# Optimization experiments

Hardware: AMD Instinct MI355X
Metric: run time of the kernel (lower is better)

The kernel has to match this reference:

```python
import jax, jax.numpy as jnp
import numpy as np

S = 8          # num_slots
DSLOT = 128    # slot_dim
D_IN = 768     # input feature dim
ITERS = 3      # slot_att_iter
RES = 21       # 336 // 16
NGRID = RES * RES   # 441 grid positions
NTOK = 441          # tokens kept per frame (no drop here)
NFRAME = 2
F_ = 2 * NFRAME + 1  # 5 frames per clip
CLIPS = 8
B = CLIPS * F_       # 40
SIGMA = 5.0
SCALE = DSLOT ** -0.5
EPS = 1e-8


def layernorm(x, g, b):
    m = x.mean(-1, keepdims=True)
    v = ((x - m) ** 2).mean(-1, keepdims=True)
    return (x - m) * jax.lax.rsqrt(v + 1e-5) * g + b


def setup_inputs() -> dict:
    key = jax.random.key(0)
    ks = iter(jax.random.split(key, 64))
    def nrm(shape, s=0.02):
        return jax.random.normal(next(ks), shape, jnp.float32) * s
    xs = jnp.linspace(-1.0, 1.0, RES)
    ys = jnp.linspace(-1.0, 1.0, RES)
    gx, gy = jnp.meshgrid(xs, ys)  # indexing='xy' as in torch
    abs_grid = jnp.stack([gx.ravel(), gy.ravel()], axis=-1)  # [NGRID, 2]
    return {
        "inputs": jax.random.normal(next(ks), (B, NTOK, D_IN), jnp.float32),
        "token_indices": jnp.sort(jax.random.randint(next(ks), (B, NTOK), 0, NGRID), axis=-1),
        "abs_grid": abs_grid,
        "slots_init": nrm((1, S, DSLOT), 0.1),
        "S_p_init": nrm((1, S, 1, 2), 0.02),
        "S_s_init": jax.random.uniform(next(ks), (1, S, 1, 2), jnp.float32, 0.3, 0.7),
        "WQ": nrm((DSLOT, DSLOT)), "ln_g": jnp.ones((DSLOT,)), "ln_b": jnp.zeros((DSLOT,)),
        "gru_w_ih": nrm((DSLOT, 3 * DSLOT)), "gru_w_hh": nrm((DSLOT, 3 * DSLOT)),
        "gru_b_ih": jnp.zeros((3 * DSLOT,)), "gru_b_hh": jnp.zeros((3 * DSLOT,)),
        "mlp_ln_g": jnp.ones((DSLOT,)), "mlp_ln_b": jnp.zeros((DSLOT,)),
        "mlp_w1": nrm((DSLOT, 4 * DSLOT)), "mlp_b1": jnp.zeros((4 * DSLOT,)),
        "mlp_w2": nrm((4 * DSLOT, DSLOT)), "mlp_b2": jnp.zeros((DSLOT,)),
        "WK": nrm((DSLOT, DSLOT)), "WV": nrm((DSLOT, DSLOT)),
        "Wg": nrm((2, DSLOT)), "bg": jnp.zeros((DSLOT,)),
        "Wf1": nrm((DSLOT, DSLOT)), "bf1": jnp.zeros((DSLOT,)),
        "Wf2": nrm((DSLOT, DSLOT)), "bf2": jnp.zeros((DSLOT,)),
        "im_ln1_g": jnp.ones((D_IN,)), "im_ln1_b": jnp.zeros((D_IN,)),
        "im_w1": nrm((D_IN, D_IN)), "im_b1": jnp.zeros((D_IN,)),
        "im_w2": nrm((D_IN, DSLOT)), "im_b2": jnp.zeros((DSLOT,)),
        "im_ln2_g": jnp.ones((DSLOT,)), "im_ln2_b": jnp.zeros((DSLOT,)),
        "fin_w": nrm((DSLOT, DSLOT)), "fin_b": jnp.zeros((DSLOT,)),
    }


def _forward(inputs, token_indices, abs_grid, slots_init, S_p_init, S_s_init,
             WQ, ln_g, ln_b, gru_w_ih, gru_w_hh, gru_b_ih, gru_b_hh,
             mlp_ln_g, mlp_ln_b, mlp_w1, mlp_b1, mlp_w2, mlp_b2,
             WK, WV, Wg, bg, Wf1, bf1, Wf2, bf2,
             im_ln1_g, im_ln1_b, im_w1, im_b1, im_w2, im_b2, im_ln2_g, im_ln2_b,
             fin_w, fin_b):
    Bb = inputs.shape[0]
    # initial_mlp: LN -> Linear -> ReLU -> Linear -> LN
    x = layernorm(inputs, im_ln1_g, im_ln1_b)
    x = jax.nn.relu(x @ im_w1 + im_b1)
    x = x @ im_w2 + im_b2
    x = layernorm(x, im_ln2_g, im_ln2_b)          # [B, N, Dslot]
    # K/V projections of inputs are slot-independent; compute once.
    Kx = x @ WK                                    # [B, N, Dslot]
    Vx = x @ WV
    ag = abs_grid[token_indices]                   # [B, N, 2] per-batch gather
    slots = jnp.broadcast_to(slots_init, (Bb, S, DSLOT))
    S_p = jnp.broadcast_to(S_p_init, (Bb, S, 1, 2))
    S_s = jnp.broadcast_to(S_s_init, (Bb, S, 1, 2))

    def f_net(z):  # f = Linear -> ReLU -> Linear
        return jax.nn.relu(z @ Wf1 + bf1) @ Wf2 + bf2

    attn = None
    for t in range(ITERS + 1):
        slots_prev = slots
        sn = layernorm(slots, ln_g, ln_b)
        rel = (ag[:, None] - S_p) / (S_s * SIGMA)  # [B, S, N, 2]
        gr = rel @ Wg + bg                          # [B, S, N, Dslot]
        k = f_net(Kx[:, None] + gr)
        v = f_net(Vx[:, None] + gr)
        q = sn @ WQ                                 # [B, S, Dslot]
        dots = jnp.einsum('bsd,bsjd->bsj', q, k) * SCALE
        attn = jax.nn.softmax(dots, axis=1) + EPS   # softmax over slots
        attn = attn / attn.sum(-1, keepdims=True)   # renormalize over tokens
        updates = jnp.einsum('bsjd,bsj->bsd', v, attn)
        S_p = jnp.einsum('bjd,bsj->bsd', ag, attn)[:, :, None, :]
        S_s = jnp.sqrt(jnp.einsum('bsjd,bsj->bsd', (ag[:, None] - S_p) ** 2, attn))[:, :, None, :]
        if t != ITERS:
            # torch GRUCell
            xg = updates.reshape(-1, DSLOT)
            hg = slots_prev.reshape(-1, DSLOT)
            gi = xg @ gru_w_ih + gru_b_ih
            gh = hg @ gru_w_hh + gru_b_hh
            i_r, i_z, i_n = jnp.split(gi, 3, axis=-1)
            h_r, h_z, h_n = jnp.split(gh, 3, axis=-1)
            r = jax.nn.sigmoid(i_r + h_r)
            z = jax.nn.sigmoid(i_z + h_z)
            n = jnp.tanh(i_n + r * h_n)
            slots = ((1.0 - z) * n + z * hg).reshape(Bb, S, DSLOT)
            # residual pre-LN MLP (dropout is identity in eval)
            y = layernorm(slots, mlp_ln_g, mlp_ln_b)
            y = jax.nn.relu(y @ mlp_w1 + mlp_b1) @ mlp_w2 + mlp_b2
            slots = slots + y
    slots = slots @ fin_w + fin_b
    attn_out = attn.reshape(-1, F_, S, NTOK)[:, NFRAME]  # center frame
    return slots, attn_out


def reference(inputs, token_indices, abs_grid, slots_init, S_p_init, S_s_init,
              WQ, ln_g, ln_b, gru_w_ih, gru_w_hh, gru_b_ih, gru_b_hh,
              mlp_ln_g, mlp_ln_b, mlp_w1, mlp_b1, mlp_w2, mlp_b2,
              WK, WV, Wg, bg, Wf1, bf1, Wf2, bf2,
              im_ln1_g, im_ln1_b, im_w1, im_b1, im_w2, im_b2, im_ln2_g, im_ln2_b,
              fin_w, fin_b):
    return _forward(inputs, token_indices, abs_grid, slots_init, S_p_init, S_s_init,
                    WQ, ln_g, ln_b, gru_w_ih, gru_w_hh, gru_b_ih, gru_b_hh,
                    mlp_ln_g, mlp_ln_b, mlp_w1, mlp_b1, mlp_w2, mlp_b2,
                    WK, WV, Wg, bg, Wf1, bf1, Wf2, bf2,
                    im_ln1_g, im_ln1_b, im_w1, im_b1, im_w2, im_b2, im_ln2_g, im_ln2_b,
                    fin_w, fin_b)
```

## Files before the change

### kernel.cpp

```cpp
#include <hip/hip_runtime.h>
#include <cstdio>

#define NB 40
#define NS 8
#define NT 441
#define DIN 768
#define DD 128
#define NTOT (NB*NT)
#define FSCALE 0.08838834764831843f

typedef short s8v __attribute__((ext_vector_type(8)));
typedef float f4v __attribute__((ext_vector_type(4)));

__device__ inline ushort f2bf(float f){
  unsigned u = __float_as_uint(f);
  unsigned r = (u + 0x7fffu + ((u >> 16) & 1u)) >> 16;
  return (ushort)r;
}
__device__ inline float bf2f(ushort h){ return __uint_as_float(((unsigned)h) << 16); }

struct PP {
  const float *inputs; const int *tok_idx; const float *abs_grid;
  const float *slots_init, *Sp_init, *Ss_init;
  const float *WQ, *ln_g, *ln_b;
  const float *gru_w_ih, *gru_w_hh, *gru_b_ih, *gru_b_hh;
  const float *mlp_ln_g, *mlp_ln_b, *mlp_w1, *mlp_b1, *mlp_w2, *mlp_b2;
  const float *WK, *WV, *Wg, *bg, *Wf1, *bf1, *Wf2, *bf2;
  const float *im_ln1_g, *im_ln1_b, *im_w1, *im_b1, *im_w2, *im_b2, *im_ln2_g, *im_ln2_b;
  const float *fin_w, *fin_b;
  float *x, *A_K, *A_V, *WKf, *WVf, *Wg1, *c1, *Wf2T;
  float *slots_g, *qw_g, *qb_g, *spss_g, *hpart_g, *a_g;
  ushort *xnh, *xnl, *hh, *hl, *W1Th, *W1Tl, *W2Th, *W2Tl;
  float *out;
};

__global__ __launch_bounds__(128) void prep_weights(PP p){
  int r = blockIdx.x, d = threadIdx.x;
  float accK = 0.f, accV = 0.f;
  for (int kk = 0; kk < DD; kk++){
    float w = p.Wf1[kk*DD + d];
    accK = fmaf(p.WK[r*DD+kk], w, accK);
    accV = fmaf(p.WV[r*DD+kk], w, accV);
  }
  p.WKf[r*DD+d] = accK; p.WVf[r*DD+d] = accV;
  if (r < 2){
    float a = 0.f;
    for (int kk = 0; kk < DD; kk++) a = fmaf(p.Wg[r*DD+kk], p.Wf1[kk*DD+d], a);
    p.Wg1[r*DD+d] = a;
  }
  if (r == 2){
    float a = 0.f;
    for (int kk = 0; kk < DD; kk++) a = fmaf(p.bg[kk], p.Wf1[kk*DD+d], a);
    p.c1[d] = a + p.bf1[d];
  }
  p.Wf2T[d*DD + r] = p.Wf2[r*DD + d];
}

__global__ __launch_bounds__(256) void transpose_split(const float* __restrict__ W,
                                                       ushort* __restrict__ WTh,
                                                       ushort* __restrict__ WTl,
                                                       int K, int N){
  __shared__ float tile[64][65];
  int tid = threadIdx.x;
  int k0 = blockIdx.x * 64, n0 = blockIdx.y * 64;
  #pragma unroll
  for (int i = 0; i < 4; i++){
    int k = i*16 + (tid >> 4);
    int n4 = (tid & 15) * 4;
    float4 v = *(const float4*)(W + (long)(k0+k)*N + n0 + n4);
    tile[k][n4+0] = v.x; tile[k][n4+1] = v.y; tile[k][n4+2] = v.z; tile[k][n4+3] = v.w;
  }
  __syncthreads();
  #pragma unroll
  for (int i = 0; i < 4; i++){
    int n = i*16 + (tid >> 4);
    int k4 = (tid & 15) * 4;
    ushort4 h4, l4;
    float v0 = tile[k4+0][n], v1 = tile[k4+1][n], v2 = tile[k4+2][n], v3 = tile[k4+3][n];
    h4.x = f2bf(v0); l4.x = f2bf(v0 - bf2f(h4.x));
    h4.y = f2bf(v1); l4.y = f2bf(v1 - bf2f(h4.y));
    h4.z = f2bf(v2); l4.z = f2bf(v2 - bf2f(h4.z));
    h4.w = f2bf(v3); l4.w = f2bf(v3 - bf2f(h4.w));
    *(ushort4*)(WTh + (long)(n0+n)*K + k0 + k4) = h4;
    *(ushort4*)(WTl + (long)(n0+n)*K + k0 + k4) = l4;
  }
}

__global__ __launch_bounds__(256) void ln1_split(PP p){
  int tok = blockIdx.x*4 + (threadIdx.x >> 6);
  int l = threadIdx.x & 63;
  const float* src = p.inputs + (long)tok*DIN;
  float4 v[3];
  float s = 0.f, s2 = 0.f;
  #pragma unroll
  for (int pp = 0; pp < 3; pp++){
    v[pp] = *(const float4*)(src + pp*256 + l*4);
    s  += v[pp].x + v[pp].y + v[pp].z + v[pp].w;
    s2 += v[pp].x*v[pp].x + v[pp].y*v[pp].y + v[pp].z*v[pp].z + v[pp].w*v[pp].w;
  }
  #pragma unroll
  for (int m = 1; m < 64; m <<= 1){ s += __shfl_xor(s, m); s2 += __shfl_xor(s2, m); }
  float mean = s*(1.f/DIN), var = s2*(1.f/DIN) - mean*mean;
  float rstd = rsqrtf(var + 1e-5f);
  #pragma unroll
  for (int pp = 0; pp < 3; pp++){
    int idx = pp*256 + l*4;
    float4 g = *(const float4*)(p.im_ln1_g + idx);
    float4 b = *(const float4*)(p.im_ln1_b + idx);
    float y0 = (v[pp].x-mean)*rstd*g.x + b.x;
    float y1 = (v[pp].y-mean)*rstd*g.y + b.y;
    float y2 = (v[pp].z-mean)*rstd*g.z + b.z;
    float y3 = (v[pp].w-mean)*rstd*g.w + b.w;
    ushort4 h4, l4;
    h4.x = f2bf(y0); l4.x = f2bf(y0 - bf2f(h4.x));
    h4.y = f2bf(y1); l4.y = f2bf(y1 - bf2f(h4.y));
    h4.z = f2bf(y2); l4.z = f2bf(y2 - bf2f(h4.z));
    h4.w = f2bf(y3); l4.w = f2bf(y3 - bf2f(h4.w));
    *(ushort4*)(p.xnh + (long)tok*DIN + idx) = h4;
    *(ushort4*)(p.xnl + (long)tok*DIN + idx) = l4;
  }
}

__global__ __launch_bounds__(256) void gemm1_128(PP p){
  __shared__ __align__(16) ushort As[2][128][40];
  __shared__ __align__(16) ushort Bs[2][128][40];
  int id = blockIdx.x;
  int xcd = id & 7, idx = id >> 3;
  int m_t = xcd + 8*(idx/6), n_t = idx % 6;
  if (m_t >= 138) return;
  int m0 = m_t*128, n0 = n_t*128;
  int tid = threadIdx.x;
  int w = tid >> 6, lane = tid & 63;
  int wm = w >> 1, wn = w & 1;
  f4v acc[4][4];
  #pragma unroll
  for (int mf = 0; mf < 4; mf++)
    #pragma unroll
    for (int nf = 0; nf < 4; nf++) acc[mf][nf] = (f4v)(0.f);

  for (int kb = 0; kb < DIN; kb += 32){
    __syncthreads();
    #pragma unroll
    for (int i = 0; i < 4; i++){
      int c = tid + i*256;
      int s = c >> 9, rem = c & 511;
      int r = rem >> 2, kg = rem & 3;
      int gr = min(m0 + r, NTOT-1);
      const float4 va = *(const float4*)((s ? p.xnl : p.xnh) + (long)gr*DIN + kb + kg*8);
      *(float4*)(&As[s][r][kg*8]) = va;
      const float4 vb = *(const float4*)((s ? p.W1Tl : p.W1Th) + (long)(n0 + r)*DIN + kb + kg*8);
      *(float4*)(&Bs[s][r][kg*8]) = vb;
    }
    __syncthreads();
    int kg = lane >> 4, rA = lane & 15;
    s8v a0[4], a1[4], b0[4], b1[4];
    #pragma unroll
    for (int mf = 0; mf < 4; mf++){
      a0[mf] = *(const s8v*)(&As[0][wm*64 + mf*16 + rA][kg*8]);
      a1[mf] = *(const s8v*)(&As[1][wm*64 + mf*16 + rA][kg*8]);
    }
    #pragma unroll
    for (int nf = 0; nf < 4; nf++){
      b0[nf] = *(const s8v*)(&Bs[0][wn*64 + nf*16 + rA][kg*8]);
      b1[nf] = *(const s8v*)(&Bs[1][wn*64 + nf*16 + rA][kg*8]);
    }
    #pragma unroll
    for (int mf = 0; mf < 4; mf++)
      #pragma unroll
      for (int nf = 0; nf < 4; nf++){
        acc[mf][nf] = __builtin_amdgcn_mfma_f32_16x16x32_bf16(a0[mf], b0[nf], acc[mf][nf], 0, 0, 0);
        acc[mf][nf] = __builtin_amdgcn_mfma_f32_16x16x32_bf16(a0[mf], b1[nf], acc[mf][nf], 0, 0, 0);
        acc[mf][nf] = __builtin_amdgcn_mfma_f32_16x16x32_bf16(a1[mf], b0[nf], acc[mf][nf], 0, 0, 0);
      }
  }

  int rbase = (lane >> 4) * 4, cn = lane & 15;
  #pragma unroll
  for (int mf = 0; mf < 4; mf++)
    #pragma unroll
    for (int nf = 0; nf < 4; nf++){
      int n = n0 + wn*64 + nf*16 + cn;
      float bs = p.im_b1[n];
      #pragma unroll
      for (int r = 0; r < 4; r++){
        int m = m0 + wm*64 + mf*16 + rbase + r;
        if (m < NTOT){
          float v = fmaxf(acc[mf][nf][r] + bs, 0.f);
          ushort h = f2bf(v);
          p.hh[(long)m*DIN + n] = h;
          p.hl[(long)m*DIN + n] = f2bf(v - bf2f(h));
        }
      }
    }
}

__global__ __launch_bounds__(256) void gemm_split2(
    const ushort* __restrict__ Ah, const ushort* __restrict__ Al,
    const ushort* __restrict__ Bh, const ushort* __restrict__ Bl,
    const float* __restrict__ bias,
    float* __restrict__ Xout, const float* __restrict__ g2, const float* __restrict__ b2,
    int M)
{
  __shared__ __align__(16) char smemc[64*132*4];
  ushort* As = (ushort*)smemc;
  ushort* Bs = (ushort*)(smemc + 10240);
  int tid = threadIdx.x;
  int n0 = blockIdx.x * 128, m0 = blockIdx.y * 64;
  int w = tid >> 6, lane = tid & 63;
  f4v acc[4][2];
  #pragma unroll
  for (int mf = 0; mf < 4; mf++)
    #pragma unroll
    for (int nf = 0; nf < 2; nf++) acc[mf][nf] = (f4v)(0.f);

  for (int kb = 0; kb < DIN; kb += 32){
    __syncthreads();
    #pragma unroll
    for (int i = 0; i < 2; i++){
      int c = tid + i*256;
      int s = c >> 8, r = (c >> 2) & 63, kg = c & 3;
      int gr = min(m0 + r, M-1);
      const float4 va = *(const float4*)((s ? Al : Ah) + (long)gr*DIN + kb + kg*8);
      *(float4*)(As + s*2560 + r*40 + kg*8) = va;
    }
    #pragma unroll
    for (int i = 0; i < 4; i++){
      int c = tid + i*256;
      int s = c >> 9, r = (c >> 2) & 127, kg = c & 3;
      const float4 vb = *(const float4*)((s ? Bl : Bh) + (long)(n0 + r)*DIN + kb + kg*8);
      *(float4*)(Bs + s*5120 + r*40 + kg*8) = vb;
    }
    __syncthreads();
    int kg = lane >> 4, rA = lane & 15;
    s8v a0[4], a1[4], b0[2], b1[2];
    #pragma unroll
    for (int mf = 0; mf < 4; mf++){
      a0[mf] = *(const s8v*)(As +        (mf*16 + rA)*40 + kg*8);
      a1[mf] = *(const s8v*)(As + 2560 + (mf*16 + rA)*40 + kg*8);
    }
    #pragma unroll
    for (int nf = 0; nf < 2; nf++){
      int rb = w*32 + nf*16 + rA;
      b0[nf] = *(const s8v*)(Bs +        rb*40 + kg*8);
      b1[nf] = *(const s8v*)(Bs + 5120 + rb*40 + kg*8);
    }
    #pragma unroll
    for (int mf = 0; mf < 4; mf++)
      #pragma unroll
      for (int nf = 0; nf < 2; nf++){
        acc[mf][nf] = __builtin_amdgcn_mfma_f32_16x16x32_bf16(a0[mf], b0[nf], acc[mf][nf], 0, 0, 0);
        acc[mf][nf] = __builtin_amdgcn_mfma_f32_16x16x32_bf16(a0[mf], b1[nf], acc[mf][nf], 0, 0, 0);
        acc[mf][nf] = __builtin_amdgcn_mfma_f32_16x16x32_bf16(a1[mf], b0[nf], acc[mf][nf], 0, 0, 0);
      }
  }

  int rbase = (lane >> 4) * 4, cn = lane & 15;
  __syncthreads();
  float* Dl = (float*)smemc;
  #pragma unroll
  for (int mf = 0; mf < 4; mf++)
    #pragma unroll
    for (int nf = 0; nf < 2; nf++){
      int n = w*32 + nf*16 + cn;
      float bs = bias[n];
      #pragma unroll
      for (int r = 0; r < 4; r++)
        Dl[(mf*16 + rbase + r)*132 + n] = acc[mf][nf][r] + bs;
    }
  __syncthreads();
  for (int rr = 0; rr < 16; rr++){
    int row = w*16 + rr;
    float e0 = Dl[row*132 + lane], e1 = Dl[row*132 + 64 + lane];
    float s = e0 + e1, s2 = e0*e0 + e1*e1;
    #pragma unroll
    for (int m2 = 1; m2 < 64; m2 <<= 1){ s += __shfl_xor(s, m2); s2 += __shfl_xor(s2, m2); }
    float mean = s*(1.f/DD), var = s2*(1.f/DD) - mean*mean;
    float rstd = rsqrtf(var + 1e-5f);
    int m = m0 + row;
    if (m < M){
      Xout[(long)m*DD + lane]      = (e0-mean)*rstd*g2[lane]      + b2[lane];
      Xout[(long)m*DD + 64 + lane] = (e1-mean)*rstd*g2[64 + lane] + b2[64 + lane];
    }
  }
}

__global__ __launch_bounds__(256) void k2_proj(PP p){
  __shared__ float xt[32][132];
  int tid = threadIdx.x; int g0 = blockIdx.x * 32;
  for (int f = tid; f < 32*32; f += 256){
    int tok = f >> 5, pos = (f & 31) * 4;
    int gt = g0 + tok;
    float4 v = (gt < NTOT) ? *(const float4*)(p.x + (long)gt*DD + pos)
                           : make_float4(0.f,0.f,0.f,0.f);
    *(float4*)&xt[tok][pos] = v;
  }
  __syncthreads();
  int d = tid & 127, grp = tid >> 7;
  float aK[16], aV[16];
  float c1v = p.c1[d];
  #pragma unroll
  for (int t = 0; t < 16; t++){ aK[t] = c1v; aV[t] = c1v; }
  for (int kk = 0; kk < DD; kk += 4){
    float k0 = p.WKf[(kk+0)*DD+d], k1 = p.WKf[(kk+1)*DD+d], k2 = p.WKf[(kk+2)*DD+d], k3 = p.WKf[(kk+3)*DD+d];
    float v0 = p.WVf[(kk+0)*DD+d], v1 = p.WVf[(kk+1)*DD+d], v2 = p.WVf[(kk+2)*DD+d], v3 = p.WVf[(kk+3)*DD+d];
    #pragma unroll
    for (int t = 0; t < 16; t++){
      float4 xv = *(const float4*)&xt[grp*16+t][kk];
      aK[t] = fmaf(xv.x,k0, fmaf(xv.y,k1, fmaf(xv.z,k2, fmaf(xv.w,k3, aK[t]))));
      aV[t] = fmaf(xv.x,v0, fmaf(xv.y,v1, fmaf(xv.z,v2, fmaf(xv.w,v3, aV[t]))));
    }
  }
  #pragma unroll
  for (int t = 0; t < 16; t++){
    int gt = g0 + grp*16 + t;
    if (gt < NTOT){ p.A_K[(long)gt*DD+d] = aK[t]; p.A_V[(long)gt*DD+d] = aV[t]; }
  }
}

__device__ void phase0g(const PP& p, int bs, int tid, float* scr, const float* sl,
                        float Sp0, float Sp1, float Ss0, float Ss1){
  float* sn   = scr;
  float* qv   = scr + 128;
  float* part = scr + 256;
  float* red  = scr + 512;
  int o = tid & 127, h = tid >> 7;
  float v = (tid < 128) ? sl[tid] : 0.f;
  float s1 = v, s2 = v*v;
  #pragma unroll
  for (int m = 1; m < 64; m <<= 1){ s1 += __shfl_xor(s1,m); s2 += __shfl_xor(s2,m); }
  if (tid < 128 && (tid & 63) == 0){ red[(tid>>6)*2] = s1; red[(tid>>6)*2+1] = s2; }
  __syncthreads();
  float mean = (red[0]+red[2])*(1.f/128.f);
  float var  = (red[1]+red[3])*(1.f/128.f) - mean*mean;
  float rstd = rsqrtf(var + 1e-5f);
  if (tid < 128) sn[tid] = (v-mean)*rstd*p.ln_g[tid] + p.ln_b[tid];
  __syncthreads();
  float acc = 0.f;
  for (int k = 0; k < 64; k++) acc = fmaf(sn[h*64+k], p.WQ[(h*64+k)*128+o], acc);
  part[h*128+o] = acc;
  __syncthreads();
  if (tid < 128) qv[tid] = part[tid] + part[128+tid];
  __syncthreads();
  float acc2 = 0.f;
  for (int k = 0; k < 64; k++) acc2 = fmaf(qv[h*64+k], p.Wf2T[(h*64+k)*128+o], acc2);
  part[h*128+o] = acc2;
  __syncthreads();
  if (tid < 128) p.qw_g[(long)bs*128+tid] = part[tid] + part[128+tid];
  float pb = (tid < 128) ? qv[tid]*p.bf2[tid] : 0.f;
  #pragma unroll
  for (int m = 1; m < 64; m <<= 1) pb += __shfl_xor(pb,m);
  if ((tid & 63) == 0) red[4 + (tid>>6)] = pb;
  __syncthreads();
  if (tid == 0){
    p.qb_g[bs] = FSCALE*(red[4]+red[5]+red[6]+red[7]);
    p.spss_g[bs*4+0] = Sp0; p.spss_g[bs*4+1] = Sp1;
    p.spss_g[bs*4+2] = 1.f/(Ss0*5.0f); p.spss_g[bs*4+3] = 1.f/(Ss1*5.0f);
  }
}

__global__ __launch_bounds__(256) void k_init(PP p){
  __shared__ float sl[128];
  __shared__ float scr[520];
  int bs = blockIdx.x, ss = bs & 7, tid = threadIdx.x;
  if (tid < 128){
    float v = p.slots_init[ss*128+tid];
    sl[tid] = v;
    p.slots_g[(long)bs*128+tid] = v;
  }
  __syncthreads();
  phase0g(p, bs, tid, scr, sl,
          p.Sp_init[ss*2], p.Sp_init[ss*2+1], p.Ss_init[ss*2], p.Ss_init[ss*2+1]);
}

template<int LAST>
__global__ __launch_bounds__(256) void kA(PP p){
  int b = blockIdx.x / 7, tile = blockIdx.x % 7;
  int tid = threadIdx.x, wid = tid >> 6, lane = tid & 63;
  __shared__ float qws[8][132];
  __shared__ float qbs[8];
  __shared__ float spssL[32];
  __shared__ float agt[64][2];
  __shared__ float a_tile[8][64];
  __shared__ float hpartL[4][8][128];
  for (int f = tid; f < 8*128; f += 256){
    int s = f >> 7, d = f & 127;
    qws[s][(d&31)*4 + (d>>5)] = p.qw_g[((long)b*8+s)*128 + d];
  }
  if (tid < 8)  qbs[tid] = p.qb_g[b*8+tid];
  if (tid < 32) spssL[tid] = p.spss_g[b*32+tid];
  if (tid < 64){
    int j = tile*64 + tid;
    float g0 = 0.f, g1 = 0.f;
    if (j < NT){ int idx = p.tok_idx[b*NT+j]; g0 = p.abs_grid[idx*2]; g1 = p.abs_grid[idx*2+1]; }
    agt[tid][0] = g0; agt[tid][1] = g1;
  }
  __syncthreads();

  {
    int tl = lane >> 2, dg = lane & 3;
    int jtok = wid*16 + tl, j = tile*64 + jtok;
    bool valid = j < NT;
    int jc = valid ? j : 0;
    float aa[32], w0[32], w1[32];
    const float* src = p.A_K + ((long)(b*NT+jc))*DD + dg*32;
    #pragma unroll
    for (int i4 = 0; i4 < 8; i4++){
      float4 t = *(const float4*)(src + i4*4);
      aa[i4*4+0]=t.x; aa[i4*4+1]=t.y; aa[i4*4+2]=t.z; aa[i4*4+3]=t.w;
    }
    #pragma unroll
    for (int i4 = 0; i4 < 8; i4++){
      float4 t0 = *(const float4*)(p.Wg1 + dg*32 + i4*4);
      float4 t1 = *(const float4*)(p.Wg1 + DD + dg*32 + i4*4);
      w0[i4*4+0]=t0.x; w0[i4*4+1]=t0.y; w0[i4*4+2]=t0.z; w0[i4*4+3]=t0.w;
      w1[i4*4+0]=t1.x; w1[i4*4+1]=t1.y; w1[i4*4+2]=t1.z; w1[i4*4+3]=t1.w;
    }
    float ag0 = agt[jtok][0], ag1 = agt[jtok][1];
    float dv[8];
    #pragma unroll
    for (int s = 0; s < 8; s++){
      float rel0 = (ag0 - spssL[s*4+0])*spssL[s*4+2];
      float rel1 = (ag1 - spssL[s*4+1])*spssL[s*4+3];
      float acc = 0.f;
      #pragma unroll
      for (int i = 0; i < 32; i++){
        float hk = fmaxf(fmaf(rel0, w0[i], fmaf(rel1, w1[i], aa[i])), 0.f);
        acc = fmaf(hk, qws[s][i*4+dg], acc);
      }
      acc += __shfl_xor(acc, 1); acc += __shfl_xor(acc, 2);
      dv[s] = acc*FSCALE + qbs[s];
    }
    if (dg == 0){
      float m = -1e30f;
      #pragma unroll
      for (int s = 0; s < 8; s++) m = fmaxf(m, dv[s]);
      float tot = 0.f;
      #pragma unroll
      for (int s = 0; s < 8; s++){ dv[s] = expf(dv[s]-m); tot += dv[s]; }
      float inv = 1.f/tot;
      #pragma unroll
      for (int s = 0; s < 8; s++)
        a_tile[s][jtok] = valid ? (dv[s]*inv + 1e-8f) : 0.f;
    }
  }
  __syncthreads();

  #pragma unroll
  for (int si = 0; si < 2; si++){
    int s = wid*2 + si;
    float a = a_tile[s][lane];
    float g0 = agt[lane][0], g1 = agt[lane][1];
    float v0 = a, v1 = a*g0, v2 = a*g1, v3 = a*g0*g0, v4 = a*g1*g1;
    #pragma unroll
    for (int m = 1; m < 64; m <<= 1){
      v0 += __shfl_xor(v0,m); v1 += __shfl_xor(v1,m); v2 += __shfl_xor(v2,m);
      v3 += __shfl_xor(v3,m); v4 += __shfl_xor(v4,m);
    }
    if (lane == 0){
      float* st = p.hpart_g + ((long)(b*7+tile)*8 + s)*136 + 128;
      st[0]=v0; st[1]=v1; st[2]=v2; st[3]=v3; st[4]=v4;
    }
  }

  if (LAST){
    if ((b % 5) == 2){
      int clip = b/5;
      for (int f = tid; f < 8*64; f += 256){
        int s = f >> 6, jt = f & 63;
        int j = tile*64 + jt;
        if (j < NT) p.a_g[((long)clip*8 + s)*NT + j] = a_tile[s][jt];
      }
    }
    return;
  }

  {
    float sp0[8], sp1[8], si0[8], si1[8];
    #pragma unroll
    for (int s = 0; s < 8; s++){
      sp0[s]=spssL[s*4+0]; sp1[s]=spssL[s*4+1]; si0[s]=spssL[s*4+2]; si1[s]=spssL[s*4+3];
    }
    int d0 = lane, d1 = lane + 64;
    float wg0a = p.Wg1[d0], wg1a = p.Wg1[DD+d0];
    float wg0b = p.Wg1[d1], wg1b = p.Wg1[DD+d1];
    float acc0[8], acc1[8];
    #pragma unroll
    for (int s = 0; s < 8; s++){ acc0[s]=0.f; acc1[s]=0.f; }
    for (int jj = wid; jj < 64; jj += 4){
      int j = tile*64 + jj;
      if (j >= NT) continue;
      float av0 = p.A_V[((long)(b*NT+j))*DD + d0];
      float av1 = p.A_V[((long)(b*NT+j))*DD + d1];
      float g0 = agt[jj][0], g1 = agt[jj][1];
      #pragma unroll
      for (int s = 0; s < 8; s++){
        float rel0 = (g0 - sp0[s])*si0[s];
        float rel1 = (g1 - sp1[s])*si1[s];
        float a = a_tile[s][jj];
        float hv0 = fmaxf(fmaf(rel0, wg0a, fmaf(rel1, wg1a, av0)), 0.f);
        float hv1 = fmaxf(fmaf(rel0, wg0b, fmaf(rel1, wg1b, av1)), 0.f);
        acc0[s] = fmaf(a, hv0, acc0[s]);
        acc1[s] = fmaf(a, hv1, acc1[s]);
      }
    }
    #pragma unroll
    for (int s = 0; s < 8; s++){ hpartL[wid][s][d0] = acc0[s]; hpartL[wid][s][d1] = acc1[s]; }
    __syncthreads();
    for (int f = tid; f < 1024; f += 256){
      int s = f >> 7, d = f & 127;
      p.hpart_g[((long)(b*7+tile)*8 + s)*136 + d] =
        hpartL[0][s][d] + hpartL[1][s][d] + hpartL[2][s][d] + hpartL[3][s][d];
    }
  }
}

template<int LAST>
__global__ __launch_bounds__(256) void kB(PP p){
  __shared__ float red[8];
  __shared__ float sl[128];
  __shared__ float hb[128];
  __shared__ float scr[2304];
  int bs = blockIdx.x, b = bs >> 3, ss = bs & 7, tid = threadIdx.x;
  if (tid < 5){
    float v = 0.f;
    #pragma unroll
    for (int t7 = 0; t7 < 7; t7++) v += p.hpart_g[((long)(b*7+t7)*8 + ss)*136 + 128 + tid];
    red[tid] = v;
  }
  __syncthreads();
  float SA = red[0], inv = 1.f/SA;
  float Sp0 = red[1]*inv, Sp1 = red[2]*inv;
  float Ss0 = sqrtf(fmaxf(red[3]*inv - Sp0*Sp0, 0.f));
  float Ss1 = sqrtf(fmaxf(red[4]*inv - Sp1*Sp1, 0.f));

  if (LAST){
    if ((b % 5) == 2){
      int clip = b/5;
      long base = (long)NB*NS*DD + ((long)clip*8 + ss)*NT;
      const float* arow = p.a_g + ((long)clip*8 + ss)*NT;
      for (int j = tid; j < NT; j += 256) p.out[base+j] = arow[j]*inv;
    }
    if (tid < 128) sl[tid] = p.slots_g[(long)bs*128+tid];
    __syncthreads();
    int o = tid & 127, h = tid >> 7;
    float acc = 0.f;
    for (int k = 0; k < 64; k++) acc = fmaf(sl[h*64+k], p.fin_w[(h*64+k)*128+o], acc);
    scr[h*128+o] = acc;
    __syncthreads();
    if (tid < 128) p.out[(long)bs*128+tid] = p.fin_b[tid] + scr[tid] + scr[128+tid];
    return;
  }

  if (tid < 128){
    float v = 0.f;
    #pragma unroll
    for (int t7 = 0; t7 < 7; t7++) v += p.hpart_g[((long)(b*7+t7)*8 + ss)*136 + tid];
    hb[tid] = v * inv;
    sl[tid] = p.slots_g[(long)bs*128+tid];
  }
  __syncthreads();
  float* part = scr;
  float* upd  = scr + 256;
  float* gil  = scr + 384;
  float* ghl  = scr + 768;
  float* hnl  = scr + 1152;
  float* yv   = scr + 1280;
  float* h1   = scr + 1408;
  int o = tid & 127, h = tid >> 7;
  float acc2 = 0.f;
  for (int k = 0; k < 64; k++) acc2 = fmaf(hb[h*64+k], p.Wf2[(h*64+k)*128+o], acc2);
  part[h*128+o] = acc2;
  __syncthreads();
  if (tid < 128) upd[tid] = part[tid] + part[128+tid] + p.bf2[tid];
  __syncthreads();
  int oA = tid, oB = tid + 256;
  float giA = p.gru_b_ih[oA], ghA = p.gru_b_hh[oA];
  float giB = 0.f, ghB = 0.f;
  if (tid < 128){ giB = p.gru_b_ih[oB]; ghB = p.gru_b_hh[oB]; }
  for (int k = 0; k < 128; k++){
    float uk = upd[k], sk = sl[k];
    giA = fmaf(uk, p.gru_w_ih[k*384+oA], giA);
    ghA = fmaf(sk, p.gru_w_hh[k*384+oA], ghA);
    if (tid < 128){
      giB = fmaf(uk, p.gru_w_ih[k*384+oB], giB);
      ghB = fmaf(sk, p.gru_w_hh[k*384+oB], ghB);
    }
  }
  gil[oA] = giA; ghl[oA] = ghA;
  if (tid < 128){ gil[oB] = giB; ghl[oB] = ghB; }
  __syncthreads();
  float hnv = 0.f;
  if (tid < 128){
    float r = 1.f/(1.f+expf(-(gil[tid]+ghl[tid])));
    float z = 1.f/(1.f+expf(-(gil[128+tid]+ghl[128+tid])));
    float n = tanhf(gil[256+tid] + r*ghl[256+tid]);
    hnv = (1.f-z)*n + z*sl[tid];
  }
  float t1 = hnv, t2 = hnv*hnv;
  #pragma unroll
  for (int m = 1; m < 64; m <<= 1){ t1 += __shfl_xor(t1,m); t2 += __shfl_xor(t2,m); }
  if (tid < 128 && (tid & 63) == 0){ red[(tid>>6)*2] = t1; red[(tid>>6)*2+1] = t2; }
  __syncthreads();
  float mean = (red[0]+red[2])*(1.f/128.f);
  float var  = (red[1]+red[3])*(1.f/128.f) - mean*mean;
  float rstd = rsqrtf(var + 1e-5f);
  if (tid < 128){
    hnl[tid] = hnv;
    yv[tid] = (hnv-mean)*rstd*p.mlp_ln_g[tid] + p.mlp_ln_b[tid];
  }
  __syncthreads();
  float m1A = p.mlp_b1[tid], m1B = p.mlp_b1[tid+256];
  for (int k = 0; k < 128; k++){
    float y = yv[k];
    m1A = fmaf(y, p.mlp_w1[k*512+tid], m1A);
    m1B = fmaf(y, p.mlp_w1[k*512+tid+256], m1B);
  }
  h1[tid] = fmaxf(m1A, 0.f); h1[tid+256] = fmaxf(m1B, 0.f);
  __syncthreads();
  float a2 = 0.f;
  for (int kk = 0; kk < 256; kk++) a2 = fmaf(h1[h*256+kk], p.mlp_w2[(h*256+kk)*128+o], a2);
  part[h*128+o] = a2;
  __syncthreads();
  if (tid < 128){
    float sln = hnl[tid] + p.mlp_b2[tid] + part[tid] + part[128+tid];
    sl[tid] = sln;
    p.slots_g[(long)bs*128+tid] = sln;
  }
  __syncthreads();
  phase0g(p, bs, tid, scr, sl, Sp0, Sp1, Ss0, Ss1);
}

extern "C" void kernel_launch(void* const* d_in, const int* in_sizes, int n_in,
                              void* d_out, int out_size, void* d_ws, size_t ws_size,
                              hipStream_t stream){
  PP p;
  p.inputs=(const float*)d_in[0]; p.tok_idx=(const int*)d_in[1]; p.abs_grid=(const float*)d_in[2];
  p.slots_init=(const float*)d_in[3]; p.Sp_init=(const float*)d_in[4]; p.Ss_init=(const float*)d_in[5];
  p.WQ=(const float*)d_in[6]; p.ln_g=(const float*)d_in[7]; p.ln_b=(const float*)d_in[8];
  p.gru_w_ih=(const float*)d_in[9]; p.gru_w_hh=(const float*)d_in[10];
  p.gru_b_ih=(const float*)d_in[11]; p.gru_b_hh=(const float*)d_in[12];
  p.mlp_ln_g=(const float*)d_in[13]; p.mlp_ln_b=(const float*)d_in[14];
  p.mlp_w1=(const float*)d_in[15]; p.mlp_b1=(const float*)d_in[16];
  p.mlp_w2=(const float*)d_in[17]; p.mlp_b2=(const float*)d_in[18];
  p.WK=(const float*)d_in[19]; p.WV=(const float*)d_in[20]; p.Wg=(const float*)d_in[21]; p.bg=(const float*)d_in[22];
  p.Wf1=(const float*)d_in[23]; p.bf1=(const float*)d_in[24]; p.Wf2=(const float*)d_in[25]; p.bf2=(const float*)d_in[26];
  p.im_ln1_g=(const float*)d_in[27]; p.im_ln1_b=(const float*)d_in[28];
  p.im_w1=(const float*)d_in[29]; p.im_b1=(const float*)d_in[30];
  p.im_w2=(const float*)d_in[31]; p.im_b2=(const float*)d_in[32];
  p.im_ln2_g=(const float*)d_in[33]; p.im_ln2_b=(const float*)d_in[34];
  p.fin_w=(const float*)d_in[35]; p.fin_b=(const float*)d_in[36];

  float* w = (float*)d_ws;
  size_t need = 0;
  auto alloc = [&](size_t nfl){ nfl = (nfl + 3) & ~(size_t)3; float* r = w + need; need += nfl; return r; };
  p.x    = alloc((size_t)NTOT*DD);
  p.A_K  = alloc((size_t)NTOT*DD);
  p.A_V  = alloc((size_t)NTOT*DD);
  p.WKf  = alloc(DD*DD);
  p.WVf  = alloc(DD*DD);
  p.Wg1  = alloc(2*DD);
  p.c1   = alloc(DD);
  p.Wf2T = alloc(DD*DD);
  p.slots_g = alloc(320*128);
  p.qw_g    = alloc(320*128);
  p.qb_g    = alloc(320);
  p.spss_g  = alloc(320*4);
  p.hpart_g = alloc((size_t)280*8*136);
  p.a_g     = alloc((size_t)8*8*NT);
  p.xnh  = (ushort*)alloc((size_t)NTOT*DIN/2);
  p.xnl  = (ushort*)alloc((size_t)NTOT*DIN/2);
  p.hh   = (ushort*)alloc((size_t)NTOT*DIN/2);
  p.hl   = (ushort*)alloc((size_t)NTOT*DIN/2);
  p.W1Th = (ushort*)alloc((size_t)DIN*DIN/2);
  p.W1Tl = (ushort*)alloc((size_t)DIN*DIN/2);
  p.W2Th = (ushort*)alloc((size_t)DD*DIN/2);
  p.W2Tl = (ushort*)alloc((size_t)DD*DIN/2);
  p.out = (float*)d_out;
  if (ws_size < need*sizeof(float)){
    fprintf(stderr, "kernel_launch: ws too small (%zu < %zu)\n", ws_size, need*sizeof(float));
    return;
  }

  prep_weights<<<dim3(DD), dim3(128), 0, stream>>>(p);
  transpose_split<<<dim3(DIN/64, DIN/64), dim3(256), 0, stream>>>(p.im_w1, p.W1Th, p.W1Tl, DIN, DIN);
  transpose_split<<<dim3(DIN/64, DD/64), dim3(256), 0, stream>>>(p.im_w2, p.W2Th, p.W2Tl, DIN, DD);
  ln1_split<<<dim3(NTOT/4), dim3(256), 0, stream>>>(p);
  gemm1_128<<<dim3(832), dim3(256), 0, stream>>>(p);
  gemm_split2<<<dim3(1, (NTOT+63)/64), dim3(256), 0, stream>>>(
      p.hh, p.hl, p.W2Th, p.W2Tl, p.im_b2,
      p.x, p.im_ln2_g, p.im_ln2_b, NTOT);
  k2_proj<<<dim3((NTOT+31)/32), dim3(256), 0, stream>>>(p);
  k_init<<<dim3(320), dim3(256), 0, stream>>>(p);

  for (int t = 0; t < 3; t++){
    kA<0><<<dim3(NB*7), dim3(256), 0, stream>>>(p);
    kB<0><<<dim3(320), dim3(256), 0, stream>>>(p);
  }
  kA<1><<<dim3(NB*7), dim3(256), 0, stream>>>(p);
  kB<1><<<dim3(320), dim3(256), 0, stream>>>(p);
}
```

Before: 461.6 us.

## Fuse LN2 and K/V projection into GEMM2 epilogue using split-bf16 MFMA

The second input-MLP GEMM now applies LayerNorm in its epilogue and immediately projects the normalized rows through the fused K/V weights with split-bf16 MFMA. This removes the fp32 x round trip and the separate scalar k2_proj kernel. Weight prep now writes transposed hi/lo bf16 copies of the fused K/V weights. The two transposes are merged into one launch, and slot init is folded into the LN1 kernel as extra blocks, cutting launch count. The cost is 68KB of dynamic shared memory per GEMM2 block, which limits occupancy, plus the K/V weights being read straight from global memory.

```diff
diff --git a/kernel.cpp b/kernel.cpp
--- a/kernel.cpp
+++ b/kernel.cpp
@@ -28,9 +28,10 @@
   const float *WK, *WV, *Wg, *bg, *Wf1, *bf1, *Wf2, *bf2;
   const float *im_ln1_g, *im_ln1_b, *im_w1, *im_b1, *im_w2, *im_b2, *im_ln2_g, *im_ln2_b;
   const float *fin_w, *fin_b;
-  float *x, *A_K, *A_V, *WKf, *WVf, *Wg1, *c1, *Wf2T;
+  float *A_K, *A_V, *Wg1, *c1, *Wf2T;
   float *slots_g, *qw_g, *qb_g, *spss_g, *hpart_g, *a_g;
   ushort *xnh, *xnl, *hh, *hl, *W1Th, *W1Tl, *W2Th, *W2Tl;
+  ushort *WKfTh, *WKfTl, *WVfTh, *WVfTl;
   float *out;
 };
 
@@ -42,7 +43,9 @@
     accK = fmaf(p.WK[r*DD+kk], w, accK);
     accV = fmaf(p.WV[r*DD+kk], w, accV);
   }
-  p.WKf[r*DD+d] = accK; p.WVf[r*DD+d] = accV;
+  ushort hk = f2bf(accK), hv = f2bf(accV);
+  p.WKfTh[d*DD + r] = hk; p.WKfTl[d*DD + r] = f2bf(accK - bf2f(hk));
+  p.WVfTh[d*DD + r] = hv; p.WVfTl[d*DD + r] = f2bf(accV - bf2f(hv));
   if (r < 2){
     float a = 0.f;
     for (int kk = 0; kk < DD; kk++) a = fmaf(p.Wg[r*DD+kk], p.Wf1[kk*DD+d], a);
@@ -56,13 +59,13 @@
   p.Wf2T[d*DD + r] = p.Wf2[r*DD + d];
 }
 
-__global__ __launch_bounds__(256) void transpose_split(const float* __restrict__ W,
-                                                       ushort* __restrict__ WTh,
-                                                       ushort* __restrict__ WTl,
-                                                       int K, int N){
+__global__ __launch_bounds__(256) void transpose_both(PP p){
   __shared__ float tile[64][65];
+  int t = blockIdx.x;
+  const float* W; ushort *WTh, *WTl; int N, k0, n0;
+  if (t < 144){ W = p.im_w1; WTh = p.W1Th; WTl = p.W1Tl; N = 768; k0 = (t/12)*64; n0 = (t%12)*64; }
+  else { t -= 144; W = p.im_w2; WTh = p.W2Th; WTl = p.W2Tl; N = 128; k0 = (t/2)*64; n0 = (t&1)*64; }
   int tid = threadIdx.x;
-  int k0 = blockIdx.x * 64, n0 = blockIdx.y * 64;
   #pragma unroll
   for (int i = 0; i < 4; i++){
     int k = i*16 + (tid >> 4);
@@ -81,43 +84,98 @@
     h4.y = f2bf(v1); l4.y = f2bf(v1 - bf2f(h4.y));
     h4.z = f2bf(v2); l4.z = f2bf(v2 - bf2f(h4.z));
     h4.w = f2bf(v3); l4.w = f2bf(v3 - bf2f(h4.w));
-    *(ushort4*)(WTh + (long)(n0+n)*K + k0 + k4) = h4;
-    *(ushort4*)(WTl + (long)(n0+n)*K + k0 + k4) = l4;
-  }
-}
-
-__global__ __launch_bounds__(256) void ln1_split(PP p){
-  int tok = blockIdx.x*4 + (threadIdx.x >> 6);
-  int l = threadIdx.x & 63;
-  const float* src = p.inputs + (long)tok*DIN;
-  float4 v[3];
-  float s = 0.f, s2 = 0.f;
-  #pragma unroll
-  for (int pp = 0; pp < 3; pp++){
-    v[pp] = *(const float4*)(src + pp*256 + l*4);
-    s  += v[pp].x + v[pp].y + v[pp].z + v[pp].w;
-    s2 += v[pp].x*v[pp].x + v[pp].y*v[pp].y + v[pp].z*v[pp].z + v[pp].w*v[pp].w;
-  }
-  #pragma unroll
-  for (int m = 1; m < 64; m <<= 1){ s += __shfl_xor(s, m); s2 += __shfl_xor(s2, m); }
-  float mean = s*(1.f/DIN), var = s2*(1.f/DIN) - mean*mean;
+    *(ushort4*)(WTh + (long)(n0+n)*DIN + k0 + k4) = h4;
+    *(ushort4*)(WTl + (long)(n0+n)*DIN + k0 + k4) = l4;
+  }
+}
+
+__device__ void phase0g(const PP& p, int bs, int tid, float* scr, const float* sl,
+                        float Sp0, float Sp1, float Ss0, float Ss1){
+  float* sn   = scr;
+  float* qv   = scr + 128;
+  float* part = scr + 256;
+  float* red  = scr + 512;
+  int o = tid & 127, h = tid >> 7;
+  float v = (tid < 128) ? sl[tid] : 0.f;
+  float s1 = v, s2 = v*v;
+  #pragma unroll
+  for (int m = 1; m < 64; m <<= 1){ s1 += __shfl_xor(s1,m); s2 += __shfl_xor(s2,m); }
+  if (tid < 128 && (tid & 63) == 0){ red[(tid>>6)*2] = s1; red[(tid>>6)*2+1] = s2; }
+  __syncthreads();
+  float mean = (red[0]+red[2])*(1.f/128.f);
+  float var  = (red[1]+red[3])*(1.f/128.f) - mean*mean;
   float rstd = rsqrtf(var + 1e-5f);
-  #pragma unroll
-  for (int pp = 0; pp < 3; pp++){
-    int idx = pp*256 + l*4;
-    float4 g = *(const float4*)(p.im_ln1_g + idx);
-    float4 b = *(const float4*)(p.im_ln1_b + idx);
-    float y0 = (v[pp].x-mean)*rstd*g.x + b.x;
-    float y1 = (v[pp].y-mean)*rstd*g.y + b.y;
-    float y2 = (v[pp].z-mean)*rstd*g.z + b.z;
-    float y3 = (v[pp].w-mean)*rstd*g.w + b.w;
-    ushort4 h4, l4;
-    h4.x = f2bf(y0); l4.x = f2bf(y0 - bf2f(h4.x));
-    h4.y = f2bf(y1); l4.y = f2bf(y1 - bf2f(h4.y));
-    h4.z = f2bf(y2); l4.z = f2bf(y2 - bf2f(h4.z));
-    h4.w = f2bf(y3); l4.w = f2bf(y3 - bf2f(h4.w));
-    *(ushort4*)(p.xnh + (long)tok*DIN + idx) = h4;
-    *(ushort4*)(p.xnl + (long)tok*DIN + idx) = l4;
+  if (tid < 128) sn[tid] = (v-mean)*rstd*p.ln_g[tid] + p.ln_b[tid];
+  __syncthreads();
+  float acc = 0.f;
+  for (int k = 0; k < 64; k++) acc = fmaf(sn[h*64+k], p.WQ[(h*64+k)*128+o], acc);
+  part[h*128+o] = acc;
+  __syncthreads();
+  if (tid < 128) qv[tid] = part[tid] + part[128+tid];
+  __syncthreads();
+  float acc2 = 0.f;
+  for (int k = 0; k < 64; k++) acc2 = fmaf(qv[h*64+k], p.Wf2T[(h*64+k)*128+o], acc2);
+  part[h*128+o] = acc2;
+  __syncthreads();
+  if (tid < 128) p.qw_g[(long)bs*128+tid] = part[tid] + part[128+tid];
+  float pb = (tid < 128) ? qv[tid]*p.bf2[tid] : 0.f;
+  #pragma unroll
+  for (int m = 1; m < 64; m <<= 1) pb += __shfl_xor(pb,m);
+  if ((tid & 63) == 0) red[4 + (tid>>6)] = pb;
+  __syncthreads();
+  if (tid == 0){
+    p.qb_g[bs] = FSCALE*(red[4]+red[5]+red[6]+red[7]);
+    p.spss_g[bs*4+0] = Sp0; p.spss_g[bs*4+1] = Sp1;
+    p.spss_g[bs*4+2] = 1.f/(Ss0*5.0f); p.spss_g[bs*4+3] = 1.f/(Ss1*5.0f);
+  }
+}
+
+__global__ __launch_bounds__(256) void ln1_init(PP p){
+  __shared__ float sl[128];
+  __shared__ float scr[520];
+  if (blockIdx.x < 4410){
+    int tok = blockIdx.x*4 + (threadIdx.x >> 6);
+    int l = threadIdx.x & 63;
+    const float* src = p.inputs + (long)tok*DIN;
+    float4 v[3];
+    float s = 0.f, s2 = 0.f;
+    #pragma unroll
+    for (int pp = 0; pp < 3; pp++){
+      v[pp] = *(const float4*)(src + pp*256 + l*4);
+      s  += v[pp].x + v[pp].y + v[pp].z + v[pp].w;
+      s2 += v[pp].x*v[pp].x + v[pp].y*v[pp].y + v[pp].z*v[pp].z + v[pp].w*v[pp].w;
+    }
+    #pragma unroll
+    for (int m = 1; m < 64; m <<= 1){ s += __shfl_xor(s, m); s2 += __shfl_xor(s2, m); }
+    float mean = s*(1.f/DIN), var = s2*(1.f/DIN) - mean*mean;
+    float rstd = rsqrtf(var + 1e-5f);
+    #pragma unroll
+    for (int pp = 0; pp < 3; pp++){
+      int idx = pp*256 + l*4;
+      float4 g = *(const float4*)(p.im_ln1_g + idx);
+      float4 b = *(const float4*)(p.im_ln1_b + idx);
+      float y0 = (v[pp].x-mean)*rstd*g.x + b.x;
+      float y1 = (v[pp].y-mean)*rstd*g.y + b.y;
+      float y2 = (v[pp].z-mean)*rstd*g.z + b.z;
+      float y3 = (v[pp].w-mean)*rstd*g.w + b.w;
+      ushort4 h4, l4;
+      h4.x = f2bf(y0); l4.x = f2bf(y0 - bf2f(h4.x));
+      h4.y = f2bf(y1); l4.y = f2bf(y1 - bf2f(h4.y));
+      h4.z = f2bf(y2); l4.z = f2bf(y2 - bf2f(h4.z));
+      h4.w = f2bf(y3); l4.w = f2bf(y3 - bf2f(h4.w));
+      *(ushort4*)(p.xnh + (long)tok*DIN + idx) = h4;
+      *(ushort4*)(p.xnl + (long)tok*DIN + idx) = l4;
+    }
+  } else {
+    int bs = blockIdx.x - 4410, ss = bs & 7, tid = threadIdx.x;
+    if (tid < 128){
+      float v = p.slots_init[ss*128+tid];
+      sl[tid] = v;
+      p.slots_g[(long)bs*128+tid] = v;
+    }
+    __syncthreads();
+    phase0g(p, bs, tid, scr, sl,
+            p.Sp_init[ss*2], p.Sp_init[ss*2+1], p.Ss_init[ss*2], p.Ss_init[ss*2+1]);
   }
 }
 
@@ -194,19 +252,15 @@
     }
 }
 
-__global__ __launch_bounds__(256) void gemm_split2(
-    const ushort* __restrict__ Ah, const ushort* __restrict__ Al,
-    const ushort* __restrict__ Bh, const ushort* __restrict__ Bl,
-    const float* __restrict__ bias,
-    float* __restrict__ Xout, const float* __restrict__ g2, const float* __restrict__ b2,
-    int M)
-{
-  __shared__ __align__(16) char smemc[64*132*4];
-  ushort* As = (ushort*)smemc;
-  ushort* Bs = (ushort*)(smemc + 10240);
-  int tid = threadIdx.x;
-  int n0 = blockIdx.x * 128, m0 = blockIdx.y * 64;
-  int w = tid >> 6, lane = tid & 63;
+__global__ __launch_bounds__(256) void gemm2_fused(PP p){
+  extern __shared__ __align__(16) char smem[];
+  ushort* As = (ushort*)smem;
+  ushort* Bs = (ushort*)(smem + 10240);
+  float*  Dl = (float*)smem;
+  ushort* xsh = (ushort*)(smem + 33792);
+  ushort* xsl = (ushort*)(smem + 33792 + 17408);
+  int m0 = blockIdx.x * 64;
+  int tid = threadIdx.x, w = tid >> 6, lane = tid & 63;
   f4v acc[4][2];
   #pragma unroll
   for (int mf = 0; mf < 4; mf++)
@@ -219,15 +273,15 @@
     for (int i = 0; i < 2; i++){
       int c = tid + i*256;
       int s = c >> 8, r = (c >> 2) & 63, kg = c & 3;
-      int gr = min(m0 + r, M-1);
-      const float4 va = *(const float4*)((s ? Al : Ah) + (long)gr*DIN + kb + kg*8);
+      int gr = min(m0 + r, NTOT-1);
+      const float4 va = *(const float4*)((s ? p.hl : p.hh) + (long)gr*DIN + kb + kg*8);
       *(float4*)(As + s*2560 + r*40 + kg*8) = va;
     }
     #pragma unroll
     for (int i = 0; i < 4; i++){
       int c = tid + i*256;
       int s = c >> 9, r = (c >> 2) & 127, kg = c & 3;
-      const float4 vb = *(const float4*)((s ? Bl : Bh) + (long)(n0 + r)*DIN + kb + kg*8);
+      const float4 vb = *(const float4*)((s ? p.W2Tl : p.W2Th) + (long)r*DIN + kb + kg*8);
       *(float4*)(Bs + s*5120 + r*40 + kg*8) = vb;
     }
     __syncthreads();
@@ -256,13 +310,12 @@
 
   int rbase = (lane >> 4) * 4, cn = lane & 15;
   __syncthreads();
-  float* Dl = (float*)smemc;
   #pragma unroll
   for (int mf = 0; mf < 4; mf++)
     #pragma unroll
     for (int nf = 0; nf < 2; nf++){
       int n = w*32 + nf*16 + cn;
-      float bs = bias[n];
+      float bs = p.im_b2[n];
       #pragma unroll
       for (int r = 0; r < 4; r++)
         Dl[(mf*16 + rbase + r)*132 + n] = acc[mf][nf][r] + bs;
@@ -276,100 +329,49 @@
     for (int m2 = 1; m2 < 64; m2 <<= 1){ s += __shfl_xor(s, m2); s2 += __shfl_xor(s2, m2); }
     float mean = s*(1.f/DD), var = s2*(1.f/DD) - mean*mean;
     float rstd = rsqrtf(var + 1e-5f);
-    int m = m0 + row;
-    if (m < M){
-      Xout[(long)m*DD + lane]      = (e0-mean)*rstd*g2[lane]      + b2[lane];
-      Xout[(long)m*DD + 64 + lane] = (e1-mean)*rstd*g2[64 + lane] + b2[64 + lane];
-    }
-  }
-}
-
-__global__ __launch_bounds__(256) void k2_proj(PP p){
-  __shared__ float xt[32][132];
-  int tid = threadIdx.x; int g0 = blockIdx.x * 32;
-  for (int f = tid; f < 32*32; f += 256){
-    int tok = f >> 5, pos = (f & 31) * 4;
-    int gt = g0 + tok;
-    float4 v = (gt < NTOT) ? *(const float4*)(p.x + (long)gt*DD + pos)
-                           : make_float4(0.f,0.f,0.f,0.f);
-    *(float4*)&xt[tok][pos] = v;
-  }
-  __syncthreads();
-  int d = tid & 127, grp = tid >> 7;
-  float aK[16], aV[16];
-  float c1v = p.c1[d];
-  #pragma unroll
-  for (int t = 0; t < 16; t++){ aK[t] = c1v; aV[t] = c1v; }
-  for (int kk = 0; kk < DD; kk += 4){
-    float k0 = p.WKf[(kk+0)*DD+d], k1 = p.WKf[(kk+1)*DD+d], k2 = p.WKf[(kk+2)*DD+d], k3 = p.WKf[(kk+3)*DD+d];
-    float v0 = p.WVf[(kk+0)*DD+d], v1 = p.WVf[(kk+1)*DD+d], v2 = p.WVf[(kk+2)*DD+d], v3 = p.WVf[(kk+3)*DD+d];
-    #pragma unroll
-    for (int t = 0; t < 16; t++){
-      float4 xv = *(const float4*)&xt[grp*16+t][kk];
-      aK[t] = fmaf(xv.x,k0, fmaf(xv.y,k1, fmaf(xv.z,k2, fmaf(xv.w,k3, aK[t]))));
-      aV[t] = fmaf(xv.x,v0, fmaf(xv.y,v1, fmaf(xv.z,v2, fmaf(xv.w,v3, aV[t]))));
-    }
-  }
-  #pragma unroll
-  for (int t = 0; t < 16; t++){
-    int gt = g0 + grp*16 + t;
-    if (gt < NTOT){ p.A_K[(long)gt*DD+d] = aK[t]; p.A_V[(long)gt*DD+d] = aV[t]; }
-  }
-}
-
-__device__ void phase0g(const PP& p, int bs, int tid, float* scr, const float* sl,
-                        float Sp0, float Sp1, float Ss0, float Ss1){
-  float* sn   = scr;
-  float* qv   = scr + 128;
-  float* part = scr + 256;
-  float* red  = scr + 512;
-  int o = tid & 127, h = tid >> 7;
-  float v = (tid < 128) ? sl[tid] : 0.f;
-  float s1 = v, s2 = v*v;
-  #pragma unroll
-  for (int m = 1; m < 64; m <<= 1){ s1 += __shfl_xor(s1,m); s2 += __shfl_xor(s2,m); }
-  if (tid < 128 && (tid & 63) == 0){ red[(tid>>6)*2] = s1; red[(tid>>6)*2+1] = s2; }
-  __syncthreads();
-  float mean = (red[0]+red[2])*(1.f/128.f);
-  float var  = (red[1]+red[3])*(1.f/128.f) - mean*mean;
-  float rstd = rsqrtf(var + 1e-5f);
-  if (tid < 128) sn[tid] = (v-mean)*rstd*p.ln_g[tid] + p.ln_b[tid];
-  __syncthreads();
-  float acc = 0.f;
-  for (int k = 0; k < 64; k++) acc = fmaf(sn[h*64+k], p.WQ[(h*64+k)*128+o], acc);
-  part[h*128+o] = acc;
-  __syncthreads();
-  if (tid < 128) qv[tid] = part[tid] + part[128+tid];
-  __syncthreads();
-  float acc2 = 0.f;
-  for (int k = 0; k < 64; k++) acc2 = fmaf(qv[h*64+k], p.Wf2T[(h*64+k)*128+o], acc2);
-  part[h*128+o] = acc2;
-  __syncthreads();
-  if (tid < 128) p.qw_g[(long)bs*128+tid] = part[tid] + part[128+tid];
-  float pb = (tid < 128) ? qv[tid]*p.bf2[tid] : 0.f;
-  #pragma unroll
-  for (int m = 1; m < 64; m <<= 1) pb += __shfl_xor(pb,m);
-  if ((tid & 63) == 0) red[4 + (tid>>6)] = pb;
-  __syncthreads();
-  if (tid == 0){
-    p.qb_g[bs] = FSCALE*(red[4]+red[5]+red[6]+red[7]);
-    p.spss_g[bs*4+0] = Sp0; p.spss_g[bs*4+1] = Sp1;
-    p.spss_g[bs*4+2] = 1.f/(Ss0*5.0f); p.spss_g[bs*4+3] = 1.f/(Ss1*5.0f);
-  }
-}
-
-__global__ __launch_bounds__(256) void k_init(PP p){
-  __shared__ float sl[128];
-  __shared__ float scr[520];
-  int bs = blockIdx.x, ss = bs & 7, tid = threadIdx.x;
-  if (tid < 128){
-    float v = p.slots_init[ss*128+tid];
-    sl[tid] = v;
-    p.slots_g[(long)bs*128+tid] = v;
-  }
-  __syncthreads();
-  phase0g(p, bs, tid, scr, sl,
-          p.Sp_init[ss*2], p.Sp_init[ss*2+1], p.Ss_init[ss*2], p.Ss_init[ss*2+1]);
+    float x0 = (e0-mean)*rstd*p.im_ln2_g[lane]    + p.im_ln2_b[lane];
+    float x1 = (e1-mean)*rstd*p.im_ln2_g[64+lane] + p.im_ln2_b[64+lane];
+    ushort h0 = f2bf(x0), h1 = f2bf(x1);
+    xsh[row*136 + lane]      = h0;  xsl[row*136 + lane]      = f2bf(x0 - bf2f(h0));
+    xsh[row*136 + 64 + lane] = h1;  xsl[row*136 + 64 + lane] = f2bf(x1 - bf2f(h1));
+  }
+  __syncthreads();
+  int kg = lane >> 4, rA = lane & 15;
+  f4v aK[8], aV[8];
+  #pragma unroll
+  for (int nf = 0; nf < 8; nf++){ aK[nf] = (f4v)(0.f); aV[nf] = (f4v)(0.f); }
+  #pragma unroll
+  for (int kb2 = 0; kb2 < 4; kb2++){
+    s8v ah = *(const s8v*)&xsh[(w*16+rA)*136 + kb2*32 + kg*8];
+    s8v al = *(const s8v*)&xsl[(w*16+rA)*136 + kb2*32 + kg*8];
+    #pragma unroll
+    for (int nf = 0; nf < 8; nf++){
+      int n = nf*16 + rA;
+      s8v bh = *(const s8v*)(p.WKfTh + n*DD + kb2*32 + kg*8);
+      s8v bl = *(const s8v*)(p.WKfTl + n*DD + kb2*32 + kg*8);
+      aK[nf] = __builtin_amdgcn_mfma_f32_16x16x32_bf16(ah, bh, aK[nf], 0, 0, 0);
+      aK[nf] = __builtin_amdgcn_mfma_f32_16x16x32_bf16(ah, bl, aK[nf], 0, 0, 0);
+      aK[nf] = __builtin_amdgcn_mfma_f32_16x16x32_bf16(al, bh, aK[nf], 0, 0, 0);
+      s8v ch = *(const s8v*)(p.WVfTh + n*DD + kb2*32 + kg*8);
+      s8v cl = *(const s8v*)(p.WVfTl + n*DD + kb2*32 + kg*8);
+      aV[nf] = __builtin_amdgcn_mfma_f32_16x16x32_bf16(ah, ch, aV[nf], 0, 0, 0);
+      aV[nf] = __builtin_amdgcn_mfma_f32_16x16x32_bf16(ah, cl, aV[nf], 0, 0, 0);
+      aV[nf] = __builtin_amdgcn_mfma_f32_16x16x32_bf16(al, ch, aV[nf], 0, 0, 0);
+    }
+  }
+  #pragma unroll
+  for (int nf = 0; nf < 8; nf++){
+    int n = nf*16 + cn;
+    float c = p.c1[n];
+    #pragma unroll
+    for (int r = 0; r < 4; r++){
+      int m = m0 + w*16 + rbase + r;
+      if (m < NTOT){
+        p.A_K[(long)m*DD + n] = aK[nf][r] + c;
+        p.A_V[(long)m*DD + n] = aV[nf][r] + c;
+      }
+    }
+  }
 }
 
 template<int LAST>
@@ -653,11 +655,8 @@
   float* w = (float*)d_ws;
   size_t need = 0;
   auto alloc = [&](size_t nfl){ nfl = (nfl + 3) & ~(size_t)3; float* r = w + need; need += nfl; return r; };
-  p.x    = alloc((size_t)NTOT*DD);
   p.A_K  = alloc((size_t)NTOT*DD);
   p.A_V  = alloc((size_t)NTOT*DD);
-  p.WKf  = alloc(DD*DD);
-  p.WVf  = alloc(DD*DD);
   p.Wg1  = alloc(2*DD);
   p.c1   = alloc(DD);
   p.Wf2T = alloc(DD*DD);
@@ -675,6 +674,10 @@
   p.W1Tl = (ushort*)alloc((size_t)DIN*DIN/2);
   p.W2Th = (ushort*)alloc((size_t)DD*DIN/2);
   p.W2Tl = (ushort*)alloc((size_t)DD*DIN/2);
+  p.WKfTh = (ushort*)alloc(DD*DD/2);
+  p.WKfTl = (ushort*)alloc(DD*DD/2);
+  p.WVfTh = (ushort*)alloc(DD*DD/2);
+  p.WVfTl = (ushort*)alloc(DD*DD/2);
   p.out = (float*)d_out;
   if (ws_size < need*sizeof(float)){
     fprintf(stderr, "kernel_launch: ws too small (%zu < %zu)\n", ws_size, need*sizeof(float));
@@ -682,15 +685,10 @@
   }
 
   prep_weights<<<dim3(DD), dim3(128), 0, stream>>>(p);
-  transpose_split<<<dim3(DIN/64, DIN/64), dim3(256), 0, stream>>>(p.im_w1, p.W1Th, p.W1Tl, DIN, DIN);
-  transpose_split<<<dim3(DIN/64, DD/64), dim3(256), 0, stream>>>(p.im_w2, p.W2Th, p.W2Tl, DIN, DD);
-  ln1_split<<<dim3(NTOT/4), dim3(256), 0, stream>>>(p);
+  transpose_both<<<dim3(168), dim3(256), 0, stream>>>(p);
+  ln1_init<<<dim3(4730), dim3(256), 0, stream>>>(p);
   gemm1_128<<<dim3(832), dim3(256), 0, stream>>>(p);
-  gemm_split2<<<dim3(1, (NTOT+63)/64), dim3(256), 0, stream>>>(
-      p.hh, p.hl, p.W2Th, p.W2Tl, p.im_b2,
-      p.x, p.im_ln2_g, p.im_ln2_b, NTOT);
-  k2_proj<<<dim3((NTOT+31)/32), dim3(256), 0, stream>>>(p);
-  k_init<<<dim3(320), dim3(256), 0, stream>>>(p);
+  gemm2_fused<<<dim3((NTOT+63)/64), dim3(256), 68608, stream>>>(p);
 
   for (int t = 0; t < 3; t++){
     kA<0><<<dim3(NB*7), dim3(256), 0, stream>>>(p);
```

New measurement: 438.2 us. 1.05x faster.
